# Kernel tuning notes

Hardware: AMD Instinct MI355X
Metric: run time of the kernel (lower is better)

Reference implementation:

```python
import jax, jax.numpy as jnp
import numpy as np

N = 8192
F_IN = 256
F_OUT = 128
SLOPE = 0.2
NEG_INF = -9000000000000000.0


def setup_inputs() -> dict:
    key = jax.random.key(0)
    k1, k2, k3, k4, k5 = jax.random.split(key, 5)
    x = jax.random.normal(k1, (N, F_IN), dtype=jnp.float32)
    adj = jax.random.randint(k2, (N, N), 0, 2).astype(jnp.float32)
    W = jax.random.normal(k3, (F_IN, F_OUT), dtype=jnp.float32) * (1.0 / np.sqrt(F_IN))
    a_src = jax.random.normal(k4, (F_OUT,), dtype=jnp.float32) * (1.0 / np.sqrt(F_OUT))
    a_dst = jax.random.normal(k5, (F_OUT,), dtype=jnp.float32) * (1.0 / np.sqrt(F_OUT))
    return {"x": x, "adj": adj, "W": W, "a_src": a_src, "a_dst": a_dst}


def reference(x, adj, W, a_src, a_dst):
    # h: (N, F_OUT)
    h = x @ W
    f_src = h @ a_src  # (N,)
    f_dst = h @ a_dst  # (N,)
    # additive attention scores: (N, N)
    e = f_src[:, None] + f_dst[None, :]
    e = jnp.where(e >= 0, e, SLOPE * e)  # leaky_relu
    e = jnp.where(adj > 0, e, NEG_INF)
    alpha = jax.nn.softmax(e, axis=1)  # (N, N)
    return alpha @ h  # (N, F_OUT)
```

## Files before the change

kernel.cpp:

```cpp
#include <hip/hip_runtime.h>
#include <hip/hip_bf16.h>

#define NN 8192
#define FIN 256
#define FO 128
#define KSPLIT 8
#define JCHUNK 1024
#define NSTEP 16
#define GSTRIDE 260
#define L2E 1.4426950408889634f
#define C2  0.28853900817779268f

typedef __bf16 bf16x8 __attribute__((ext_vector_type(8)));
typedef __bf16 bf16x2 __attribute__((ext_vector_type(2)));
typedef float  f32x4  __attribute__((ext_vector_type(4)));

__device__ __forceinline__ void dma16(const float* g, float* l) {
  __builtin_amdgcn_global_load_lds(
      (__attribute__((address_space(1))) void*)g,
      (__attribute__((address_space(3))) void*)l, 16, 0, 0);
}

__global__ __launch_bounds__(256) void k_proj(
    const float* __restrict__ x, const float* __restrict__ W,
    const float* __restrict__ a_src, const float* __restrict__ a_dst,
    __bf16* __restrict__ Bp, float* __restrict__ f_src, float* __restrict__ f_dst)
{
  __shared__ float xs[16 * FIN];
  __shared__ float fs[16], fd[16];
  const int tid = threadIdx.x;
  const int i0 = blockIdx.x * 16;

  const float4* xg = (const float4*)(x + (size_t)i0 * FIN);
  float4* xs4 = (float4*)xs;
  #pragma unroll
  for (int t = 0; t < 4; t++) xs4[tid + 256 * t] = xg[tid + 256 * t];
  if (tid < 16) { fs[tid] = 0.f; fd[tid] = 0.f; }
  __syncthreads();

  const int cq = tid & 31;
  const int rg = tid >> 5;
  const int c0 = cq * 4;
  const int r0 = rg * 2;
  float acc0[4] = {0.f,0.f,0.f,0.f};
  float acc1[4] = {0.f,0.f,0.f,0.f};
  const float* xr0 = xs + r0 * FIN;
  const float* xr1 = xs + (r0 + 1) * FIN;

  for (int k = 0; k < FIN; k += 4) {
    float4 xa = *(const float4*)(xr0 + k);
    float4 xb = *(const float4*)(xr1 + k);
    #pragma unroll
    for (int kk = 0; kk < 4; kk++) {
      float4 wv = *(const float4*)(W + (size_t)(k + kk) * FO + c0);
      float xav = ((const float*)&xa)[kk];
      float xbv = ((const float*)&xb)[kk];
      acc0[0] += xav * wv.x; acc0[1] += xav * wv.y;
      acc0[2] += xav * wv.z; acc0[3] += xav * wv.w;
      acc1[0] += xbv * wv.x; acc1[1] += xbv * wv.y;
      acc1[2] += xbv * wv.z; acc1[3] += xbv * wv.w;
    }
  }

  float4 as = *(const float4*)(a_src + c0);
  float4 ad = *(const float4*)(a_dst + c0);
  float ps0 = acc0[0]*as.x + acc0[1]*as.y + acc0[2]*as.z + acc0[3]*as.w;
  float ps1 = acc1[0]*as.x + acc1[1]*as.y + acc1[2]*as.z + acc1[3]*as.w;
  float pd0 = acc0[0]*ad.x + acc0[1]*ad.y + acc0[2]*ad.z + acc0[3]*ad.w;
  float pd1 = acc1[0]*ad.x + acc1[1]*ad.y + acc1[2]*ad.z + acc1[3]*ad.w;
  atomicAdd(&fs[r0],     ps0);
  atomicAdd(&fs[r0 + 1], ps1);
  atomicAdd(&fd[r0],     pd0);
  atomicAdd(&fd[r0 + 1], pd1);

  const int j0 = i0 + r0;
  const int kg = j0 >> 5;
  const int q  = (j0 >> 3) & 3;
  const int t0 = j0 & 7;
  #pragma unroll
  for (int c = 0; c < 4; c++) {
    const int n = c0 + c;
    bf16x2 v;
    v[0] = (__bf16)acc0[c];
    v[1] = (__bf16)acc1[c];
    size_t idx = ((size_t)(kg * 8 + (n >> 4)) * 64 + q * 16 + (n & 15)) * 8 + t0;
    *(bf16x2*)(Bp + idx) = v;
  }
  __syncthreads();
  if (tid < 16) { f_src[i0 + tid] = fs[tid]; f_dst[i0 + tid] = fd[tid]; }
}

__global__ __launch_bounds__(256, 2) void k_attn(
    const float* __restrict__ adj, const __bf16* __restrict__ Bp,
    const float* __restrict__ f_src, const float* __restrict__ f_dst,
    float* __restrict__ num, float* __restrict__ lsum)
{
  __shared__ float G1[JCHUNK];
  __shared__ float G2[JCHUNK];
  __shared__ __align__(16) float atile[4][2][8 * GSTRIDE];

  const int tid = threadIdx.x;
  const int rb = blockIdx.x >> 3;
  const int ks = blockIdx.x & 7;
  const int i0 = rb * 128;
  const int jbase = ks * JCHUNK;

  #pragma unroll
  for (int t = 0; t < 4; t++) {
    int j = tid + t * 256;
    float d = f_dst[jbase + j];
    G1[j] = __builtin_amdgcn_exp2f(d * L2E);
    G2[j] = __builtin_amdgcn_exp2f(d * C2);
  }

  const int w = tid >> 6;
  const int lane = tid & 63;
  const int m = lane & 15;
  const int q = lane >> 4;
  const int wbase = i0 + w * 32;

  float F1[2], F2[2];
  #pragma unroll
  for (int mt = 0; mt < 2; mt++) {
    float s = f_src[wbase + mt * 16 + m];
    F1[mt] = __builtin_amdgcn_exp2f(s * L2E);
    F2[mt] = __builtin_amdgcn_exp2f(s * C2);
  }

  f32x4 acc[2][8];
  #pragma unroll
  for (int mt = 0; mt < 2; mt++)
    #pragma unroll
    for (int nt = 0; nt < 8; nt++) acc[mt][nt] = (f32x4){0.f, 0.f, 0.f, 0.f};
  float psum[2] = {0.f, 0.f};

  const float* gsrc = adj + (size_t)(wbase + (lane >> 4)) * NN + jbase + (lane & 15) * 4;
  float* tw0 = &atile[w][0][0];
  float* tw1 = &atile[w][1][0];

#define ISSUE(buf, step)                                                      \
  {                                                                           \
    const float* gs = gsrc + (step) * 64;                                     \
    float* lb = (buf) ? tw1 : tw0;                                            \
    _Pragma("unroll")                                                         \
    for (int g = 0; g < 8; g++)                                               \
      dma16(gs + (size_t)g * 4 * NN, lb + g * GSTRIDE);                       \
  }

  ISSUE(0, 0)

  for (int step = 0; step < NSTEP; ++step) {
    const int buf = step & 1;
    if (step + 1 < NSTEP) ISSUE(buf ^ 1, step + 1)
    __syncthreads();

    const float* tb = buf ? tw1 : tw0;
    #pragma unroll
    for (int kg = 0; kg < 2; kg++) {
      const int jj = step * 64 + kg * 32 + q * 8;
      float4 u0 = *(const float4*)(G1 + jj);
      float4 u1 = *(const float4*)(G1 + jj + 4);
      float4 v0 = *(const float4*)(G2 + jj);
      float4 v1 = *(const float4*)(G2 + jj + 4);

      bf16x8 af[2];
      #pragma unroll
      for (int mt = 0; mt < 2; mt++) {
        const int r = mt * 16 + m;
        const float* ap = tb + (r >> 2) * GSTRIDE + (r & 3) * 64 + kg * 32 + q * 8;
        float4 a0 = *(const float4*)ap;
        float4 a1 = *(const float4*)(ap + 4);
        const float f1 = F1[mt], f2 = F2[mt];
        float p0 = (a0.x > 0.f) ? fmaxf(f1 * u0.x, f2 * v0.x) : 0.f;
        float p1 = (a0.y > 0.f) ? fmaxf(f1 * u0.y, f2 * v0.y) : 0.f;
        float p2 = (a0.z > 0.f) ? fmaxf(f1 * u0.z, f2 * v0.z) : 0.f;
        float p3 = (a0.w > 0.f) ? fmaxf(f1 * u0.w, f2 * v0.w) : 0.f;
        float p4 = (a1.x > 0.f) ? fmaxf(f1 * u1.x, f2 * v1.x) : 0.f;
        float p5 = (a1.y > 0.f) ? fmaxf(f1 * u1.y, f2 * v1.y) : 0.f;
        float p6 = (a1.z > 0.f) ? fmaxf(f1 * u1.z, f2 * v1.z) : 0.f;
        float p7 = (a1.w > 0.f) ? fmaxf(f1 * u1.w, f2 * v1.w) : 0.f;
        psum[mt] += ((p0 + p1) + (p2 + p3)) + ((p4 + p5) + (p6 + p7));
        bf16x8 a;
        a[0] = (__bf16)p0; a[1] = (__bf16)p1; a[2] = (__bf16)p2; a[3] = (__bf16)p3;
        a[4] = (__bf16)p4; a[5] = (__bf16)p5; a[6] = (__bf16)p6; a[7] = (__bf16)p7;
        af[mt] = a;
      }

      const __bf16* bsrc = Bp + (size_t)(ks * 32 + step * 2 + kg) * 4096 + lane * 8;
      #pragma unroll
      for (int nt = 0; nt < 8; nt++) {
        bf16x8 bfrag = *(const bf16x8*)(bsrc + nt * 512);
        acc[0][nt] = __builtin_amdgcn_mfma_f32_16x16x32_bf16(af[0], bfrag, acc[0][nt], 0, 0, 0);
        acc[1][nt] = __builtin_amdgcn_mfma_f32_16x16x32_bf16(af[1], bfrag, acc[1][nt], 0, 0, 0);
      }
    }
  }
#undef ISSUE

  #pragma unroll
  for (int mt = 0; mt < 2; mt++) {
    float p = psum[mt];
    p += __shfl_xor(p, 16);
    p += __shfl_xor(p, 32);
    if (lane < 16) atomicAdd(&lsum[wbase + mt * 16 + lane], p);
  }

  #pragma unroll
  for (int mt = 0; mt < 2; mt++) {
    const int rb0 = wbase + mt * 16 + q * 4;
    #pragma unroll
    for (int nt = 0; nt < 8; nt++) {
      #pragma unroll
      for (int r = 0; r < 4; r++) {
        atomicAdd(&num[(size_t)(rb0 + r) * FO + nt * 16 + m], acc[mt][nt][r]);
      }
    }
  }
}

__global__ __launch_bounds__(256) void k_div(
    const float* __restrict__ num, const float* __restrict__ lsum,
    float* __restrict__ out)
{
  int idx = blockIdx.x * 256 + threadIdx.x;
  float4 v = ((const float4*)num)[idx];
  float inv = 1.0f / lsum[idx >> 5];
  float4 o;
  o.x = v.x * inv; o.y = v.y * inv; o.z = v.z * inv; o.w = v.w * inv;
  ((float4*)out)[idx] = o;
}

extern "C" void kernel_launch(void* const* d_in, const int* in_sizes, int n_in,
                              void* d_out, int out_size, void* d_ws, size_t ws_size,
                              hipStream_t stream) {
  const float* x     = (const float*)d_in[0];
  const float* adj   = (const float*)d_in[1];
  const float* W     = (const float*)d_in[2];
  const float* a_src = (const float*)d_in[3];
  const float* a_dst = (const float*)d_in[4];
  float* out = (float*)d_out;

  char* ws = (char*)d_ws;
  __bf16* Bp   = (__bf16*)ws;
  float* f_src = (float*)(ws + 2097152);
  float* f_dst = (float*)(ws + 2097152 + 32768);
  float* num   = (float*)(ws + 2097152 + 65536);
  float* lsum  = (float*)(ws + 2097152 + 65536 + 4194304);

  hipMemsetAsync(num, 0, 4194304 + 32768, stream);
  hipLaunchKernelGGL(k_proj, dim3(512), dim3(256), 0, stream,
                     x, W, a_src, a_dst, Bp, f_src, f_dst);
  hipLaunchKernelGGL(k_attn, dim3(512), dim3(256), 0, stream,
                     adj, Bp, f_src, f_dst, num, lsum);
  hipLaunchKernelGGL(k_div, dim3(1024), dim3(256), 0, stream,
                     num, lsum, out);
}
```

Baseline: 448.4 us.

## Fuse split-K reduction and normalization into attention kernel with in-block K split

Each block now owns 32 rows and its 8 waves split the full column range, so partial sums are reduced through shared-memory atomics instead of global atomics. The separate memset and division kernel go away, and the output is normalized inside the attention kernel. Adjacency is read with direct nontemporal register loads and software prefetch in place of LDS DMA double buffering. The exp tables are precomputed once in the projection kernel, and block size becomes 512. The trade-off is fewer blocks (256), more registers held for prefetch, and a large LDS footprint (full 8192-entry G tables) that may limit occupancy.

```diff
diff --git a/kernel.cpp b/kernel.cpp
--- a/kernel.cpp
+++ b/kernel.cpp
@@ -4,10 +4,8 @@
 #define NN 8192
 #define FIN 256
 #define FO 128
-#define KSPLIT 8
-#define JCHUNK 1024
-#define NSTEP 16
-#define GSTRIDE 260
+#define WCH 1024
+#define WSTEP 16
 #define L2E 1.4426950408889634f
 #define C2  0.28853900817779268f
 
@@ -15,16 +13,11 @@
 typedef __bf16 bf16x2 __attribute__((ext_vector_type(2)));
 typedef float  f32x4  __attribute__((ext_vector_type(4)));
 
-__device__ __forceinline__ void dma16(const float* g, float* l) {
-  __builtin_amdgcn_global_load_lds(
-      (__attribute__((address_space(1))) void*)g,
-      (__attribute__((address_space(3))) void*)l, 16, 0, 0);
-}
-
 __global__ __launch_bounds__(256) void k_proj(
     const float* __restrict__ x, const float* __restrict__ W,
     const float* __restrict__ a_src, const float* __restrict__ a_dst,
-    __bf16* __restrict__ Bp, float* __restrict__ f_src, float* __restrict__ f_dst)
+    __bf16* __restrict__ Bp, float* __restrict__ f_src,
+    float* __restrict__ g1, float* __restrict__ g2)
 {
   __shared__ float xs[16 * FIN];
   __shared__ float fs[16], fd[16];
@@ -87,42 +80,51 @@
     *(bf16x2*)(Bp + idx) = v;
   }
   __syncthreads();
-  if (tid < 16) { f_src[i0 + tid] = fs[tid]; f_dst[i0 + tid] = fd[tid]; }
+  if (tid < 16) {
+    float d = fd[tid];
+    f_src[i0 + tid] = fs[tid];
+    g1[i0 + tid] = __builtin_amdgcn_exp2f(d * L2E);
+    g2[i0 + tid] = __builtin_amdgcn_exp2f(d * C2);
+  }
 }
 
-__global__ __launch_bounds__(256, 2) void k_attn(
+__global__ __launch_bounds__(512, 2) void k_attn(
     const float* __restrict__ adj, const __bf16* __restrict__ Bp,
-    const float* __restrict__ f_src, const float* __restrict__ f_dst,
-    float* __restrict__ num, float* __restrict__ lsum)
+    const float* __restrict__ f_src, const float* __restrict__ g1,
+    const float* __restrict__ g2, float* __restrict__ out)
 {
-  __shared__ float G1[JCHUNK];
-  __shared__ float G2[JCHUNK];
-  __shared__ __align__(16) float atile[4][2][8 * GSTRIDE];
-
+  __shared__ float G1s[NN];
+  __shared__ float G2s[NN];
+  __shared__ float accbuf[32 * FO];
+  __shared__ float lred[32];
   const int tid = threadIdx.x;
-  const int rb = blockIdx.x >> 3;
-  const int ks = blockIdx.x & 7;
-  const int i0 = rb * 128;
-  const int jbase = ks * JCHUNK;
-
-  #pragma unroll
-  for (int t = 0; t < 4; t++) {
-    int j = tid + t * 256;
-    float d = f_dst[jbase + j];
-    G1[j] = __builtin_amdgcn_exp2f(d * L2E);
-    G2[j] = __builtin_amdgcn_exp2f(d * C2);
-  }
+  const int i0 = blockIdx.x * 32;
+
+  {
+    const float4* s1 = (const float4*)g1;
+    const float4* s2 = (const float4*)g2;
+    float4* d1 = (float4*)G1s;
+    float4* d2 = (float4*)G2s;
+    #pragma unroll
+    for (int t = 0; t < 4; t++) {
+      d1[tid + 512 * t] = s1[tid + 512 * t];
+      d2[tid + 512 * t] = s2[tid + 512 * t];
+    }
+  }
+  ((float4*)accbuf)[tid]       = (float4){0.f, 0.f, 0.f, 0.f};
+  ((float4*)accbuf)[tid + 512] = (float4){0.f, 0.f, 0.f, 0.f};
+  if (tid < 32) lred[tid] = 0.f;
 
   const int w = tid >> 6;
   const int lane = tid & 63;
   const int m = lane & 15;
   const int q = lane >> 4;
-  const int wbase = i0 + w * 32;
+  const int jbase = w * WCH;
 
   float F1[2], F2[2];
   #pragma unroll
   for (int mt = 0; mt < 2; mt++) {
-    float s = f_src[wbase + mt * 16 + m];
+    float s = f_src[i0 + mt * 16 + m];
     F1[mt] = __builtin_amdgcn_exp2f(s * L2E);
     F2[mt] = __builtin_amdgcn_exp2f(s * C2);
   }
@@ -134,42 +136,47 @@
     for (int nt = 0; nt < 8; nt++) acc[mt][nt] = (f32x4){0.f, 0.f, 0.f, 0.f};
   float psum[2] = {0.f, 0.f};
 
-  const float* gsrc = adj + (size_t)(wbase + (lane >> 4)) * NN + jbase + (lane & 15) * 4;
-  float* tw0 = &atile[w][0][0];
-  float* tw1 = &atile[w][1][0];
-
-#define ISSUE(buf, step)                                                      \
-  {                                                                           \
-    const float* gs = gsrc + (step) * 64;                                     \
-    float* lb = (buf) ? tw1 : tw0;                                            \
-    _Pragma("unroll")                                                         \
-    for (int g = 0; g < 8; g++)                                               \
-      dma16(gs + (size_t)g * 4 * NN, lb + g * GSTRIDE);                       \
-  }
-
-  ISSUE(0, 0)
-
-  for (int step = 0; step < NSTEP; ++step) {
-    const int buf = step & 1;
-    if (step + 1 < NSTEP) ISSUE(buf ^ 1, step + 1)
-    __syncthreads();
-
-    const float* tb = buf ? tw1 : tw0;
-    #pragma unroll
-    for (int kg = 0; kg < 2; kg++) {
-      const int jj = step * 64 + kg * 32 + q * 8;
-      float4 u0 = *(const float4*)(G1 + jj);
-      float4 u1 = *(const float4*)(G1 + jj + 4);
-      float4 v0 = *(const float4*)(G2 + jj);
-      float4 v1 = *(const float4*)(G2 + jj + 4);
+  const float* adjp[2];
+  adjp[0] = adj + (size_t)(i0 + m) * NN + jbase + q * 8;
+  adjp[1] = adjp[0] + (size_t)16 * NN;
+  const __bf16* bb = Bp + (size_t)(jbase >> 5) * 4096 + lane * 8;
+
+  __syncthreads();
+
+  f32x4 c[2][2][2];
+  #pragma unroll
+  for (int mt = 0; mt < 2; mt++) {
+    c[mt][0][0] = __builtin_nontemporal_load((const f32x4*)(adjp[mt] + 0));
+    c[mt][0][1] = __builtin_nontemporal_load((const f32x4*)(adjp[mt] + 4));
+    c[mt][1][0] = __builtin_nontemporal_load((const f32x4*)(adjp[mt] + 32));
+    c[mt][1][1] = __builtin_nontemporal_load((const f32x4*)(adjp[mt] + 36));
+  }
+
+  for (int st = 0; st < WSTEP; ++st) {
+    f32x4 n[2][2][2];
+    if (st < WSTEP - 1) {
+      #pragma unroll
+      for (int mt = 0; mt < 2; mt++) {
+        const float* ap = adjp[mt] + (st + 1) * 64;
+        n[mt][0][0] = __builtin_nontemporal_load((const f32x4*)(ap + 0));
+        n[mt][0][1] = __builtin_nontemporal_load((const f32x4*)(ap + 4));
+        n[mt][1][0] = __builtin_nontemporal_load((const f32x4*)(ap + 32));
+        n[mt][1][1] = __builtin_nontemporal_load((const f32x4*)(ap + 36));
+      }
+    }
+    #pragma unroll
+    for (int g = 0; g < 2; ++g) {
+      const int jj = jbase + st * 64 + g * 32 + q * 8;
+      float4 u0 = *(const float4*)(G1s + jj);
+      float4 u1 = *(const float4*)(G1s + jj + 4);
+      float4 v0 = *(const float4*)(G2s + jj);
+      float4 v1 = *(const float4*)(G2s + jj + 4);
 
       bf16x8 af[2];
       #pragma unroll
       for (int mt = 0; mt < 2; mt++) {
-        const int r = mt * 16 + m;
-        const float* ap = tb + (r >> 2) * GSTRIDE + (r & 3) * 64 + kg * 32 + q * 8;
-        float4 a0 = *(const float4*)ap;
-        float4 a1 = *(const float4*)(ap + 4);
+        f32x4 a0 = c[mt][g][0];
+        f32x4 a1 = c[mt][g][1];
         const float f1 = F1[mt], f2 = F2[mt];
         float p0 = (a0.x > 0.f) ? fmaxf(f1 * u0.x, f2 * v0.x) : 0.f;
         float p1 = (a0.y > 0.f) ? fmaxf(f1 * u0.y, f2 * v0.y) : 0.f;
@@ -186,48 +193,54 @@
         af[mt] = a;
       }
 
-      const __bf16* bsrc = Bp + (size_t)(ks * 32 + step * 2 + kg) * 4096 + lane * 8;
+      const __bf16* bs = bb + (size_t)(st * 2 + g) * 4096;
       #pragma unroll
       for (int nt = 0; nt < 8; nt++) {
-        bf16x8 bfrag = *(const bf16x8*)(bsrc + nt * 512);
+        bf16x8 bfrag = *(const bf16x8*)(bs + nt * 512);
         acc[0][nt] = __builtin_amdgcn_mfma_f32_16x16x32_bf16(af[0], bfrag, acc[0][nt], 0, 0, 0);
         acc[1][nt] = __builtin_amdgcn_mfma_f32_16x16x32_bf16(af[1], bfrag, acc[1][nt], 0, 0, 0);
       }
     }
-  }
-#undef ISSUE
+    if (st < WSTEP - 1) {
+      #pragma unroll
+      for (int mt = 0; mt < 2; mt++)
+        #pragma unroll
+        for (int g = 0; g < 2; g++) {
+          c[mt][g][0] = n[mt][g][0];
+          c[mt][g][1] = n[mt][g][1];
+        }
+    }
+  }
 
   #pragma unroll
   for (int mt = 0; mt < 2; mt++) {
     float p = psum[mt];
     p += __shfl_xor(p, 16);
     p += __shfl_xor(p, 32);
-    if (lane < 16) atomicAdd(&lsum[wbase + mt * 16 + lane], p);
-  }
-
-  #pragma unroll
-  for (int mt = 0; mt < 2; mt++) {
-    const int rb0 = wbase + mt * 16 + q * 4;
+    if (lane < 16) atomicAdd(&lred[mt * 16 + lane], p);
+  }
+
+  #pragma unroll
+  for (int mt = 0; mt < 2; mt++) {
     #pragma unroll
     for (int nt = 0; nt < 8; nt++) {
       #pragma unroll
       for (int r = 0; r < 4; r++) {
-        atomicAdd(&num[(size_t)(rb0 + r) * FO + nt * 16 + m], acc[mt][nt][r]);
-      }
-    }
-  }
-}
-
-__global__ __launch_bounds__(256) void k_div(
-    const float* __restrict__ num, const float* __restrict__ lsum,
-    float* __restrict__ out)
-{
-  int idx = blockIdx.x * 256 + threadIdx.x;
-  float4 v = ((const float4*)num)[idx];
-  float inv = 1.0f / lsum[idx >> 5];
-  float4 o;
-  o.x = v.x * inv; o.y = v.y * inv; o.z = v.z * inv; o.w = v.w * inv;
-  ((float4*)out)[idx] = o;
+        atomicAdd(&accbuf[(mt * 16 + q * 4 + r) * FO + nt * 16 + m], acc[mt][nt][r]);
+      }
+    }
+  }
+  __syncthreads();
+
+  #pragma unroll
+  for (int t = 0; t < 2; t++) {
+    const int idx = tid + t * 512;
+    const float inv = 1.0f / lred[idx >> 5];
+    float4 v = ((const float4*)accbuf)[idx];
+    float4 o;
+    o.x = v.x * inv; o.y = v.y * inv; o.z = v.z * inv; o.w = v.w * inv;
+    ((float4*)(out + (size_t)i0 * FO))[idx] = o;
+  }
 }
 
 extern "C" void kernel_launch(void* const* d_in, const int* in_sizes, int n_in,
@@ -243,15 +256,11 @@
   char* ws = (char*)d_ws;
   __bf16* Bp   = (__bf16*)ws;
   float* f_src = (float*)(ws + 2097152);
-  float* f_dst = (float*)(ws + 2097152 + 32768);
-  float* num   = (float*)(ws + 2097152 + 65536);
-  float* lsum  = (float*)(ws + 2097152 + 65536 + 4194304);
-
-  hipMemsetAsync(num, 0, 4194304 + 32768, stream);
+  float* g1    = (float*)(ws + 2097152 + 32768);
+  float* g2    = (float*)(ws + 2097152 + 65536);
+
   hipLaunchKernelGGL(k_proj, dim3(512), dim3(256), 0, stream,
-                     x, W, a_src, a_dst, Bp, f_src, f_dst);
-  hipLaunchKernelGGL(k_attn, dim3(512), dim3(256), 0, stream,
-                     adj, Bp, f_src, f_dst, num, lsum);
-  hipLaunchKernelGGL(k_div, dim3(1024), dim3(256), 0, stream,
-                     num, lsum, out);
+                     x, W, a_src, a_dst, Bp, f_src, g1, g2);
+  hipLaunchKernelGGL(k_attn, dim3(256), dim3(512), 0, stream,
+                     adj, Bp, f_src, g1, g2, out);
 }
```

Result: slower. 478.0 us (+6.6%).
